# Kernel optimization log

Measured on AMD Instinct MI355X. Metric: run time of the kernel, lower is better.

Reference implementation:

```python
import jax, jax.numpy as jnp
import numpy as np

N_NODES = 50000


def gcn_conv(x, src, dst, W, b, n_nodes):
    """PyG-style GCNConv: x' = D^-1/2 (A + I) D^-1/2 (x W) + b.
    src/dst already include self-loops."""
    h = x @ W  # [N, C_out]
    # symmetric normalization from degree (with self-loops, unit edge weight)
    deg = jax.ops.segment_sum(jnp.ones_like(dst, dtype=h.dtype), dst,
                              num_segments=n_nodes)  # [N]
    dinv = jnp.where(deg > 0, jax.lax.rsqrt(deg), 0.0)
    norm = dinv[src] * dinv[dst]  # [E]
    msg = h[src] * norm[:, None]  # gather + scale, [E, C_out]
    out = jax.ops.segment_sum(msg, dst, num_segments=n_nodes)  # scatter-add
    return out + b


def setup_inputs() -> dict:
    key = jax.random.key(0)
    k1, k2, k3, k4, k5, k6 = jax.random.split(key, 6)
    in_c, hid_c, out_c = 128, 64, 64
    x = jax.random.normal(k1, (N_NODES, in_c), dtype=jnp.float32)
    edge_index = jax.random.randint(k2, (2, 800000), 0, N_NODES, dtype=jnp.int64)
    # Glorot-ish init for weights, zeros for bias (as PyG default)
    W1 = jax.random.normal(k3, (in_c, hid_c), dtype=jnp.float32) / np.sqrt(in_c)
    b1 = jnp.zeros((hid_c,), dtype=jnp.float32)
    W2 = jax.random.normal(k4, (hid_c, out_c), dtype=jnp.float32) / np.sqrt(hid_c)
    b2 = jnp.zeros((out_c,), dtype=jnp.float32)
    return {"x": x, "edge_index": edge_index, "W1": W1, "b1": b1,
            "W2": W2, "b2": b2}


def reference(x, edge_index, W1, b1, W2, b2):
    n = x.shape[0]
    loops = jnp.arange(n, dtype=edge_index.dtype)
    src = jnp.concatenate([edge_index[0], loops])  # add self-loops
    dst = jnp.concatenate([edge_index[1], loops])
    h = gcn_conv(x, src, dst, W1, b1, n)
    h = jax.nn.relu(h)
    return gcn_conv(h, src, dst, W2, b2, n)
```

## Files before the change

### kernel.cpp

```cpp
#include <hip/hip_runtime.h>
#include <hip/hip_fp16.h>


#define C_HID 64
#define NCHUNK 512
#define ES3 768
#define ES4 768

static inline size_t alignup(size_t x) { return (x + 255) & ~(size_t)255; }

typedef __attribute__((address_space(3))) unsigned int lds_uint;
typedef __attribute__((address_space(1))) const unsigned int glob_uint;

__device__ __forceinline__ int blockScanIncl256(int v, int* wsum) {
    const int lane = threadIdx.x & 63, wav = threadIdx.x >> 6;
    int s = v;
#pragma unroll
    for (int off = 1; off < 64; off <<= 1) {
        int t = __shfl_up(s, off);
        if (lane >= off) s += t;
    }
    if (lane == 63) wsum[wav] = s;
    __syncthreads();
    if (wav == 0 && lane < 4) {
        int ws = wsum[lane];
#pragma unroll
        for (int off = 1; off < 4; off <<= 1) {
            int t = __shfl_up(ws, off);
            if (lane >= off) ws += t;
        }
        wsum[lane] = ws;
    }
    __syncthreads();
    return (wav ? wsum[wav - 1] : 0) + s;
}

template <int K>
__global__ __launch_bounds__(256) void gemm1_hist_kernel(
    const float* __restrict__ X, const float* __restrict__ W,
    const int* __restrict__ dst, __half* __restrict__ outh,
    int* __restrict__ S, int n, int E, int ePer, int nb) {
    constexpr int KP = K + 4;
    __shared__ float Xs[64 * KP];
    __shared__ float Ws[K * 64];
    __shared__ int h[1024];
    const int t = threadIdx.x;
    const int lane = t & 63;
    const int wav = t >> 6;

    if ((int)blockIdx.x < NCHUNK) {
        for (int i = t; i < nb; i += 256) h[i] = 0;
        __syncthreads();
        int beg = blockIdx.x * ePer, end = min(E, beg + ePer);
        for (int e = beg + t; e < end; e += 256)
            atomicAdd(&h[dst[e] >> 6], 1);
        __syncthreads();
        for (int b = t; b < nb; b += 256)
            S[(size_t)b * NCHUNK + blockIdx.x] = h[b];
        return;
    }

    const int row0 = ((int)blockIdx.x - NCHUNK) * 64;
    {
        const char* gb = (const char*)W;
        char* lb = (char*)Ws;
        for (int off = wav * 1024; off < K * 64 * 4; off += 4096)
            __builtin_amdgcn_global_load_lds((glob_uint*)(gb + off + lane * 16),
                                             (lds_uint*)(lb + off), 16, 0, 0);
    }
    if (row0 + 64 <= n) {
        const float4* g4 = (const float4*)(X + (size_t)row0 * K);
        for (int i = t; i < 64 * (K / 4); i += 256) {
            float4 v = g4[i];
            int r = i / (K / 4), k0 = (i % (K / 4)) * 4;
            *(float4*)&Xs[r * KP + k0] = v;
        }
    } else {
        for (int i = t; i < 64 * K; i += 256) {
            int r = i / K, k = i % K;
            Xs[r * KP + k] = (row0 + r < n) ? X[(size_t)(row0 + r) * K + k] : 0.0f;
        }
    }
    __syncthreads();

    const int tx = t & 15;
    const int ty = t >> 4;
    float acc[4][4] = {{0.f}};
#pragma unroll 2
    for (int k0 = 0; k0 < K; k0 += 4) {
        float4 a0 = *(const float4*)&Xs[(4 * ty + 0) * KP + k0];
        float4 a1 = *(const float4*)&Xs[(4 * ty + 1) * KP + k0];
        float4 a2 = *(const float4*)&Xs[(4 * ty + 2) * KP + k0];
        float4 a3 = *(const float4*)&Xs[(4 * ty + 3) * KP + k0];
        float4 b0 = *(const float4*)&Ws[(k0 + 0) * 64 + 4 * tx];
        float4 b1 = *(const float4*)&Ws[(k0 + 1) * 64 + 4 * tx];
        float4 b2 = *(const float4*)&Ws[(k0 + 2) * 64 + 4 * tx];
        float4 b3 = *(const float4*)&Ws[(k0 + 3) * 64 + 4 * tx];
        const float* ap[4] = {(const float*)&a0, (const float*)&a1,
                              (const float*)&a2, (const float*)&a3};
        const float* bp[4] = {(const float*)&b0, (const float*)&b1,
                              (const float*)&b2, (const float*)&b3};
#pragma unroll
        for (int r = 0; r < 4; ++r)
#pragma unroll
            for (int kk = 0; kk < 4; ++kk) {
                float av = ap[r][kk];
#pragma unroll
                for (int c = 0; c < 4; ++c)
                    acc[r][c] = fmaf(av, bp[kk][c], acc[r][c]);
            }
    }
#pragma unroll
    for (int r = 0; r < 4; ++r) {
        int row = row0 + 4 * ty + r;
        if (row < n) {
            __half2 p01 = __floats2half2_rn(acc[r][0], acc[r][1]);
            __half2 p23 = __floats2half2_rn(acc[r][2], acc[r][3]);
            float2 st;
            ((__half2*)&st)[0] = p01;
            ((__half2*)&st)[1] = p23;
            *(float2*)&outh[(size_t)row * 64 + 4 * tx] = st;
        }
    }
}

__global__ __launch_bounds__(256) void scan_rows_kernel(
    int* __restrict__ S, int* __restrict__ T) {
    __shared__ int wsum[4];
    const int b = blockIdx.x, t = threadIdx.x;
    int4 v = make_int4(0, 0, 0, 0);
    if (t < NCHUNK / 4) v = ((const int4*)(S + (size_t)b * NCHUNK))[t];
    int p1 = v.x + v.y, p2 = p1 + v.z, p3 = p2 + v.w;
    int incl = blockScanIncl256(p3, wsum);
    int excl = incl - p3;
    if (t < NCHUNK / 4) {
        int4 o;
        o.x = excl; o.y = excl + v.x; o.z = excl + p1; o.w = excl + p2;
        ((int4*)(S + (size_t)b * NCHUNK))[t] = o;
    }
    if (t == 0) T[b] = wsum[3];
}

__global__ __launch_bounds__(256) void scatter_kernel(
    const int* __restrict__ src, const int* __restrict__ dst, int E, int ePer,
    const int* __restrict__ S, const int* __restrict__ T,
    unsigned* __restrict__ ebuf, int nb) {
    __shared__ int tmp[1024];
    __shared__ int arr[1024];
    __shared__ int wsum[4];
    const int b = blockIdx.x, t = threadIdx.x;
    {
        int a0 = (4 * t + 0 < nb) ? T[4 * t + 0] : 0;
        int a1 = (4 * t + 1 < nb) ? T[4 * t + 1] : 0;
        int a2 = (4 * t + 2 < nb) ? T[4 * t + 2] : 0;
        int a3 = (4 * t + 3 < nb) ? T[4 * t + 3] : 0;
        int p1 = a0 + a1, p2 = p1 + a2, p3 = p2 + a3;
        int incl = blockScanIncl256(p3, wsum);
        int excl = incl - p3;
        tmp[4 * t + 0] = excl;
        tmp[4 * t + 1] = excl + a0;
        tmp[4 * t + 2] = excl + p1;
        tmp[4 * t + 3] = excl + p2;
    }
    __syncthreads();
    for (int i = t; i < nb; i += 256)
        arr[i] = S[(size_t)i * NCHUNK + b] + tmp[i];
    __syncthreads();
    int beg = b * ePer, end = min(E, beg + ePer);
    for (int e = beg + t; e < end; e += 256) {
        int d = dst[e];
        int s = src[e];
        int pos = atomicAdd(&arr[d >> 6], 1);
        ebuf[pos] = ((unsigned)s << 6) | (unsigned)(d & 63);
    }
}

__global__ __launch_bounds__(256) void build_kernel(
    const unsigned* __restrict__ ebuf, const int* __restrict__ T,
    int* __restrict__ row_ptr, float* __restrict__ dinv,
    int* __restrict__ esrc, __half* __restrict__ g1, int n, int nb) {
    __shared__ int tmp[1024];
    __shared__ int cnt[64];
    __shared__ int cur[64];
    __shared__ float dvs[64];
    __shared__ int wsum[4];
    const int b = blockIdx.x, t = threadIdx.x;
    {
        int a0 = (4 * t + 0 < nb) ? T[4 * t + 0] : 0;
        int a1 = (4 * t + 1 < nb) ? T[4 * t + 1] : 0;
        int a2 = (4 * t + 2 < nb) ? T[4 * t + 2] : 0;
        int a3 = (4 * t + 3 < nb) ? T[4 * t + 3] : 0;
        int p1 = a0 + a1, p2 = p1 + a2, p3 = p2 + a3;
        int incl = blockScanIncl256(p3, wsum);
        int excl = incl - p3;
        tmp[4 * t + 0] = excl + a0;
        tmp[4 * t + 1] = excl + p1;
        tmp[4 * t + 2] = excl + p2;
        tmp[4 * t + 3] = excl + p3;
    }
    if (t < 64) cnt[t] = 0;
    __syncthreads();
    const int ebeg = b ? tmp[b - 1] : 0;
    const int eend = tmp[b];

    for (int e = ebeg + t; e < eend; e += 256)
        atomicAdd(&cnt[ebuf[e] & 63], 1);
    __syncthreads();
    if (t < 64) {
        int deg = cnt[t];
        int s = deg;
#pragma unroll
        for (int off = 1; off < 64; off <<= 1) {
            int x = __shfl_up(s, off);
            if (t >= off) s += x;
        }
        cur[t] = ebeg + s - deg;
        float dv = rsqrtf(1.0f + (float)deg);
        dvs[t] = dv;
        int v = (b << 6) + t;
        if (v < n) {
            row_ptr[v + 1] = ebeg + s;
            dinv[v] = dv;
            if (v == 0) row_ptr[0] = 0;
        }
    }
    __syncthreads();
    for (int e = ebeg + t; e < eend; e += 256) {
        unsigned p = ebuf[e];
        int pos = atomicAdd(&cur[p & 63], 1);
        esrc[pos] = (int)(p >> 6);
    }
    {
        const int row = t >> 2, q = t & 3;
        const int v = (b << 6) + row;
        if (v < n) {
            float dv = dvs[row];
            float4* gp = (float4*)(g1 + (size_t)v * 64 + q * 16);
            float4 r0 = gp[0], r1 = gp[1];
            __half2* h0 = (__half2*)&r0;
            __half2* h1 = (__half2*)&r1;
#pragma unroll
            for (int i2 = 0; i2 < 4; ++i2) {
                float2 f0 = __half22float2(h0[i2]);
                float2 f1 = __half22float2(h1[i2]);
                h0[i2] = __floats2half2_rn(f0.x * dv, f0.y * dv);
                h1[i2] = __floats2half2_rn(f1.x * dv, f1.y * dv);
            }
            gp[0] = r0;
            gp[1] = r1;
        }
    }
}

__device__ __forceinline__ void addf4(float acc[8], const float4& r) {
    const __half2* h = (const __half2*)&r;
#pragma unroll
    for (int q = 0; q < 4; ++q) {
        float2 f = __half22float2(h[q]);
        acc[2 * q] += f.x;
        acc[2 * q + 1] += f.y;
    }
}

template <bool LDSE>
__device__ __forceinline__ void agg8_body(
    const float4* __restrict__ hs4, const int* es, const int* __restrict__ esg,
    int beg0, int beg, int end, int c8, float acc[8]) {
    int j = beg;
    for (; j + 8 <= end; j += 8) {
        int s0, s1, s2, s3, s4, s5, s6, s7;
        if (LDSE) {
            s0 = es[j];     s1 = es[j + 1]; s2 = es[j + 2]; s3 = es[j + 3];
            s4 = es[j + 4]; s5 = es[j + 5]; s6 = es[j + 6]; s7 = es[j + 7];
        } else {
            const int* p = esg + beg0 + j;
            s0 = p[0]; s1 = p[1]; s2 = p[2]; s3 = p[3];
            s4 = p[4]; s5 = p[5]; s6 = p[6]; s7 = p[7];
        }
        float4 r0 = hs4[(size_t)s0 * 8 + c8];
        float4 r1 = hs4[(size_t)s1 * 8 + c8];
        float4 r2 = hs4[(size_t)s2 * 8 + c8];
        float4 r3 = hs4[(size_t)s3 * 8 + c8];
        float4 r4 = hs4[(size_t)s4 * 8 + c8];
        float4 r5 = hs4[(size_t)s5 * 8 + c8];
        float4 r6 = hs4[(size_t)s6 * 8 + c8];
        float4 r7 = hs4[(size_t)s7 * 8 + c8];
        addf4(acc, r0); addf4(acc, r1); addf4(acc, r2); addf4(acc, r3);
        addf4(acc, r4); addf4(acc, r5); addf4(acc, r6); addf4(acc, r7);
    }
    if (j + 4 <= end) {
        int s0, s1, s2, s3;
        if (LDSE) {
            s0 = es[j]; s1 = es[j + 1]; s2 = es[j + 2]; s3 = es[j + 3];
        } else {
            const int* p = esg + beg0 + j;
            s0 = p[0]; s1 = p[1]; s2 = p[2]; s3 = p[3];
        }
        float4 r0 = hs4[(size_t)s0 * 8 + c8];
        float4 r1 = hs4[(size_t)s1 * 8 + c8];
        float4 r2 = hs4[(size_t)s2 * 8 + c8];
        float4 r3 = hs4[(size_t)s3 * 8 + c8];
        addf4(acc, r0); addf4(acc, r1); addf4(acc, r2); addf4(acc, r3);
        j += 4;
    }
    for (; j < end; ++j) {
        int s0 = LDSE ? es[j] : esg[beg0 + j];
        float4 r0 = hs4[(size_t)s0 * 8 + c8];
        addf4(acc, r0);
    }
}

__global__ __launch_bounds__(256) void agg1_gemm2_kernel(
    const __half* __restrict__ g1, const int* __restrict__ row_ptr,
    const int* __restrict__ esrc, const float* __restrict__ dinv,
    const float* __restrict__ b1, const float* __restrict__ W2,
    __half* __restrict__ g2, int n) {
    __shared__ float Bt[32][68];
    __shared__ float Ws2[64 * 64];
    __shared__ int es[ES3];
    const int t = threadIdx.x, lane = t & 63, wav = t >> 6;
    const int row0 = blockIdx.x * 32;

    const int beg0 = row_ptr[row0];
    const int end0 = row_ptr[min(row0 + 32, n)];
    const int tot = end0 - beg0;
    const bool uselds = (tot <= ES3);
    if (uselds)
        for (int i = t; i < tot; i += 256) es[i] = esrc[beg0 + i];
    __syncthreads();

    {
        const char* gb = (const char*)W2;
        char* lb = (char*)Ws2;
        for (int off = wav * 1024; off < 64 * 64 * 4; off += 4096)
            __builtin_amdgcn_global_load_lds((glob_uint*)(gb + off + lane * 16),
                                             (lds_uint*)(lb + off), 16, 0, 0);
    }

    const int g = t >> 3;
    const int c8 = t & 7;
    const int v = row0 + g;
    const float4* __restrict__ hs4 = (const float4*)g1;

    if (v < n) {
        float acc[8];
        {
            float4 raw = hs4[(size_t)v * 8 + c8];
            const __half2* hp = (const __half2*)&raw;
#pragma unroll
            for (int q = 0; q < 4; ++q) {
                float2 f = __half22float2(hp[q]);
                acc[2 * q] = f.x; acc[2 * q + 1] = f.y;
            }
        }
        const int beg = row_ptr[v] - beg0;
        const int end = row_ptr[v + 1] - beg0;
        if (uselds) agg8_body<true>(hs4, es, esrc, beg0, beg, end, c8, acc);
        else        agg8_body<false>(hs4, es, esrc, beg0, beg, end, c8, acc);
        const float dv0 = dinv[v];
        const float* bb = b1 + c8 * 8;
        float4 w0, w1;
        w0.x = fmaxf(fmaf(acc[0], dv0, bb[0]), 0.f);
        w0.y = fmaxf(fmaf(acc[1], dv0, bb[1]), 0.f);
        w0.z = fmaxf(fmaf(acc[2], dv0, bb[2]), 0.f);
        w0.w = fmaxf(fmaf(acc[3], dv0, bb[3]), 0.f);
        w1.x = fmaxf(fmaf(acc[4], dv0, bb[4]), 0.f);
        w1.y = fmaxf(fmaf(acc[5], dv0, bb[5]), 0.f);
        w1.z = fmaxf(fmaf(acc[6], dv0, bb[6]), 0.f);
        w1.w = fmaxf(fmaf(acc[7], dv0, bb[7]), 0.f);
        *(float4*)&Bt[g][c8 * 8] = w0;
        *(float4*)&Bt[g][c8 * 8 + 4] = w1;
    } else {
        *(float4*)&Bt[g][c8 * 8] = make_float4(0.f, 0.f, 0.f, 0.f);
        *(float4*)&Bt[g][c8 * 8 + 4] = make_float4(0.f, 0.f, 0.f, 0.f);
    }
    __syncthreads();

    const int tx = t & 15;
    const int ty = t >> 4;
    float a2[2][4] = {{0.f}};
#pragma unroll 2
    for (int k0 = 0; k0 < 64; k0 += 4) {
        float4 x0 = *(const float4*)&Bt[2 * ty + 0][k0];
        float4 x1 = *(const float4*)&Bt[2 * ty + 1][k0];
        float4 w0 = *(const float4*)&Ws2[(k0 + 0) * 64 + 4 * tx];
        float4 w1 = *(const float4*)&Ws2[(k0 + 1) * 64 + 4 * tx];
        float4 w2 = *(const float4*)&Ws2[(k0 + 2) * 64 + 4 * tx];
        float4 w3 = *(const float4*)&Ws2[(k0 + 3) * 64 + 4 * tx];
        const float* xp[2] = {(const float*)&x0, (const float*)&x1};
        const float* wp[4] = {(const float*)&w0, (const float*)&w1,
                              (const float*)&w2, (const float*)&w3};
#pragma unroll
        for (int r = 0; r < 2; ++r)
#pragma unroll
            for (int kk = 0; kk < 4; ++kk) {
                float av = xp[r][kk];
#pragma unroll
                for (int cc = 0; cc < 4; ++cc)
                    a2[r][cc] = fmaf(av, wp[kk][cc], a2[r][cc]);
            }
    }
#pragma unroll
    for (int r = 0; r < 2; ++r) {
        int row = row0 + 2 * ty + r;
        if (row < n) {
            float dv = dinv[row];
            __half2 p01 = __floats2half2_rn(a2[r][0] * dv, a2[r][1] * dv);
            __half2 p23 = __floats2half2_rn(a2[r][2] * dv, a2[r][3] * dv);
            float2 st;
            ((__half2*)&st)[0] = p01;
            ((__half2*)&st)[1] = p23;
            *(float2*)&g2[(size_t)row * 64 + 4 * tx] = st;
        }
    }
}

__global__ __launch_bounds__(256) void aggregate2_kernel(
    const __half* __restrict__ hs,
    const int* __restrict__ row_ptr,
    const int* __restrict__ esrc,
    const float* __restrict__ dinv,
    const float* __restrict__ bias,
    float* __restrict__ out, int n) {
    __shared__ int es[ES4];
    const int t = threadIdx.x;
    const int row0 = blockIdx.x * 32;
    const int beg0 = row_ptr[row0];
    const int end0 = row_ptr[min(row0 + 32, n)];
    const int tot = end0 - beg0;
    const bool uselds = (tot <= ES4);
    if (uselds)
        for (int i = t; i < tot; i += 256) es[i] = esrc[beg0 + i];
    __syncthreads();

    const int v = row0 + (t >> 3);
    if (v >= n) return;
    const int c8 = t & 7;
    const float4* __restrict__ hs4 = (const float4*)hs;

    float acc[8];
    {
        float4 raw = hs4[(size_t)v * 8 + c8];
        const __half2* hp = (const __half2*)&raw;
#pragma unroll
        for (int q = 0; q < 4; ++q) {
            float2 f = __half22float2(hp[q]);
            acc[2 * q] = f.x; acc[2 * q + 1] = f.y;
        }
    }

    const int beg = row_ptr[v] - beg0;
    const int end = row_ptr[v + 1] - beg0;
    if (uselds) agg8_body<true>(hs4, es, esrc, beg0, beg, end, c8, acc);
    else        agg8_body<false>(hs4, es, esrc, beg0, beg, end, c8, acc);

    float dv = dinv[v];
    float4 b0 = *(const float4*)(bias + c8 * 8);
    float4 b1v = *(const float4*)(bias + c8 * 8 + 4);
    float4 o0, o1;
    o0.x = fmaf(acc[0], dv, b0.x); o0.y = fmaf(acc[1], dv, b0.y);
    o0.z = fmaf(acc[2], dv, b0.z); o0.w = fmaf(acc[3], dv, b0.w);
    o1.x = fmaf(acc[4], dv, b1v.x); o1.y = fmaf(acc[5], dv, b1v.y);
    o1.z = fmaf(acc[6], dv, b1v.z); o1.w = fmaf(acc[7], dv, b1v.w);
    float4* op = (float4*)(out + (size_t)v * 64 + c8 * 8);
    op[0] = o0;
    op[1] = o1;
}

extern "C" void kernel_launch(void* const* d_in, const int* in_sizes, int n_in,
                              void* d_out, int out_size, void* d_ws, size_t ws_size,
                              hipStream_t stream) {
    const float* x  = (const float*)d_in[0];
    const int*   ei = (const int*)d_in[1];
    const float* W1 = (const float*)d_in[2];
    const float* b1 = (const float*)d_in[3];
    const float* W2 = (const float*)d_in[4];
    const float* b2 = (const float*)d_in[5];
    float* out = (float*)d_out;

    const int C_IN = 128;
    const int n = in_sizes[0] / C_IN;
    const int E = in_sizes[1] / 2;
    const int* src = ei;
    const int* dst = ei + E;

    const int nb = (n + 63) >> 6;
    const int ngb = (n + 63) / 64;
    const int n32 = (n + 31) / 32;
    const int ePer = (E + NCHUNK - 1) / NCHUNK;

    char* w = (char*)d_ws;
    float*    dinv    = (float*)w;    w += alignup((size_t)n * sizeof(float));
    __half*   g1      = (__half*)w;   w += alignup((size_t)n * C_HID * sizeof(__half));
    __half*   g2      = (__half*)w;   w += alignup((size_t)n * C_HID * sizeof(__half));
    int*      row_ptr = (int*)w;      w += alignup((size_t)(n + 1) * sizeof(int));
    int*      S       = (int*)w;      w += alignup((size_t)nb * NCHUNK * sizeof(int));
    int*      T       = (int*)w;      w += alignup((size_t)(nb + 1) * sizeof(int));
    unsigned* ebuf    = (unsigned*)w; w += alignup((size_t)E * sizeof(unsigned));
    int*      esrc    = (int*)w;

    gemm1_hist_kernel<128><<<NCHUNK + ngb, 256, 0, stream>>>(
        x, W1, dst, g1, S, n, E, ePer, nb);

    scan_rows_kernel<<<nb, 256, 0, stream>>>(S, T);
    scatter_kernel<<<NCHUNK, 256, 0, stream>>>(src, dst, E, ePer, S, T, ebuf, nb);
    build_kernel<<<nb, 256, 0, stream>>>(ebuf, T, row_ptr, dinv, esrc, g1, n, nb);

    agg1_gemm2_kernel<<<n32, 256, 0, stream>>>(
        g1, row_ptr, esrc, dinv, b1, W2, g2, n);

    aggregate2_kernel<<<n32, 256, 0, stream>>>(
        g2, row_ptr, esrc, dinv, b2, out, n);
}
```

Before: 161.2 us.

## Build CSR with global per-node degree atomics and direct atomic scatter

Replaces the chunked two-level counting sort (per-chunk histograms, row scan, bucketed scatter into an intermediate buffer, then per-bucket local sort) with global per-node degree atomics in the histogram pass, a single build kernel that derives row_ptr and per-node cursors, and a direct scatter using global atomics on those cursors. It removes one kernel launch, the S matrix and the intermediate ebuf round trip. In exchange it adds a memset, many contended global atomics, and a nondeterministic edge order within each row, which can change floating-point summation order.

```diff
diff --git a/kernel.cpp b/kernel.cpp
--- a/kernel.cpp
+++ b/kernel.cpp
@@ -5,7 +5,6 @@
 #define C_HID 64
 #define NCHUNK 512
 #define ES3 768
-#define ES4 768
 
 static inline size_t alignup(size_t x) { return (x + 255) & ~(size_t)255; }
 
@@ -39,7 +38,8 @@
 __global__ __launch_bounds__(256) void gemm1_hist_kernel(
     const float* __restrict__ X, const float* __restrict__ W,
     const int* __restrict__ dst, __half* __restrict__ outh,
-    int* __restrict__ S, int n, int E, int ePer, int nb) {
+    int* __restrict__ deg, int* __restrict__ T,
+    int n, int E, int ePer, int nb) {
     constexpr int KP = K + 4;
     __shared__ float Xs[64 * KP];
     __shared__ float Ws[K * 64];
@@ -52,11 +52,16 @@
         for (int i = t; i < nb; i += 256) h[i] = 0;
         __syncthreads();
         int beg = blockIdx.x * ePer, end = min(E, beg + ePer);
-        for (int e = beg + t; e < end; e += 256)
-            atomicAdd(&h[dst[e] >> 6], 1);
+        for (int e = beg + t; e < end; e += 256) {
+            int d = dst[e];
+            atomicAdd(&deg[d], 1);
+            atomicAdd(&h[d >> 6], 1);
+        }
         __syncthreads();
-        for (int b = t; b < nb; b += 256)
-            S[(size_t)b * NCHUNK + blockIdx.x] = h[b];
+        for (int b = t; b < nb; b += 256) {
+            int c = h[b];
+            if (c) atomicAdd(&T[b], c);
+        }
         return;
     }
 
@@ -124,64 +129,11 @@
     }
 }
 
-__global__ __launch_bounds__(256) void scan_rows_kernel(
-    int* __restrict__ S, int* __restrict__ T) {
-    __shared__ int wsum[4];
-    const int b = blockIdx.x, t = threadIdx.x;
-    int4 v = make_int4(0, 0, 0, 0);
-    if (t < NCHUNK / 4) v = ((const int4*)(S + (size_t)b * NCHUNK))[t];
-    int p1 = v.x + v.y, p2 = p1 + v.z, p3 = p2 + v.w;
-    int incl = blockScanIncl256(p3, wsum);
-    int excl = incl - p3;
-    if (t < NCHUNK / 4) {
-        int4 o;
-        o.x = excl; o.y = excl + v.x; o.z = excl + p1; o.w = excl + p2;
-        ((int4*)(S + (size_t)b * NCHUNK))[t] = o;
-    }
-    if (t == 0) T[b] = wsum[3];
-}
-
-__global__ __launch_bounds__(256) void scatter_kernel(
-    const int* __restrict__ src, const int* __restrict__ dst, int E, int ePer,
-    const int* __restrict__ S, const int* __restrict__ T,
-    unsigned* __restrict__ ebuf, int nb) {
+__global__ __launch_bounds__(256) void build_kernel(
+    const int* __restrict__ deg, const int* __restrict__ T,
+    int* __restrict__ row_ptr, float* __restrict__ dinv, int* __restrict__ cur,
+    __half* __restrict__ g1, int n, int nb) {
     __shared__ int tmp[1024];
-    __shared__ int arr[1024];
-    __shared__ int wsum[4];
-    const int b = blockIdx.x, t = threadIdx.x;
-    {
-        int a0 = (4 * t + 0 < nb) ? T[4 * t + 0] : 0;
-        int a1 = (4 * t + 1 < nb) ? T[4 * t + 1] : 0;
-        int a2 = (4 * t + 2 < nb) ? T[4 * t + 2] : 0;
-        int a3 = (4 * t + 3 < nb) ? T[4 * t + 3] : 0;
-        int p1 = a0 + a1, p2 = p1 + a2, p3 = p2 + a3;
-        int incl = blockScanIncl256(p3, wsum);
-        int excl = incl - p3;
-        tmp[4 * t + 0] = excl;
-        tmp[4 * t + 1] = excl + a0;
-        tmp[4 * t + 2] = excl + p1;
-        tmp[4 * t + 3] = excl + p2;
-    }
-    __syncthreads();
-    for (int i = t; i < nb; i += 256)
-        arr[i] = S[(size_t)i * NCHUNK + b] + tmp[i];
-    __syncthreads();
-    int beg = b * ePer, end = min(E, beg + ePer);
-    for (int e = beg + t; e < end; e += 256) {
-        int d = dst[e];
-        int s = src[e];
-        int pos = atomicAdd(&arr[d >> 6], 1);
-        ebuf[pos] = ((unsigned)s << 6) | (unsigned)(d & 63);
-    }
-}
-
-__global__ __launch_bounds__(256) void build_kernel(
-    const unsigned* __restrict__ ebuf, const int* __restrict__ T,
-    int* __restrict__ row_ptr, float* __restrict__ dinv,
-    int* __restrict__ esrc, __half* __restrict__ g1, int n, int nb) {
-    __shared__ int tmp[1024];
-    __shared__ int cnt[64];
-    __shared__ int cur[64];
     __shared__ float dvs[64];
     __shared__ int wsum[4];
     const int b = blockIdx.x, t = threadIdx.x;
@@ -198,38 +150,28 @@
         tmp[4 * t + 2] = excl + p2;
         tmp[4 * t + 3] = excl + p3;
     }
-    if (t < 64) cnt[t] = 0;
     __syncthreads();
     const int ebeg = b ? tmp[b - 1] : 0;
-    const int eend = tmp[b];
-
-    for (int e = ebeg + t; e < eend; e += 256)
-        atomicAdd(&cnt[ebuf[e] & 63], 1);
-    __syncthreads();
+
     if (t < 64) {
-        int deg = cnt[t];
-        int s = deg;
+        const int v = (b << 6) + t;
+        int d = (v < n) ? deg[v] : 0;
+        int s = d;
 #pragma unroll
         for (int off = 1; off < 64; off <<= 1) {
             int x = __shfl_up(s, off);
             if (t >= off) s += x;
         }
-        cur[t] = ebeg + s - deg;
-        float dv = rsqrtf(1.0f + (float)deg);
+        float dv = rsqrtf(1.0f + (float)d);
         dvs[t] = dv;
-        int v = (b << 6) + t;
         if (v < n) {
             row_ptr[v + 1] = ebeg + s;
+            cur[v] = ebeg + s - d;
             dinv[v] = dv;
             if (v == 0) row_ptr[0] = 0;
         }
     }
     __syncthreads();
-    for (int e = ebeg + t; e < eend; e += 256) {
-        unsigned p = ebuf[e];
-        int pos = atomicAdd(&cur[p & 63], 1);
-        esrc[pos] = (int)(p >> 6);
-    }
     {
         const int row = t >> 2, q = t & 3;
         const int v = (b << 6) + row;
@@ -249,6 +191,18 @@
             gp[0] = r0;
             gp[1] = r1;
         }
+    }
+}
+
+__global__ __launch_bounds__(256) void scatter_kernel(
+    const int* __restrict__ src, const int* __restrict__ dst, int E,
+    int* __restrict__ cur, int* __restrict__ esrc) {
+    const int stride = gridDim.x * 256;
+    for (int e = blockIdx.x * 256 + threadIdx.x; e < E; e += stride) {
+        int d = dst[e];
+        int s = src[e];
+        int pos = atomicAdd(&cur[d], 1);
+        esrc[pos] = s;
     }
 }
 
@@ -422,13 +376,13 @@
     const float* __restrict__ dinv,
     const float* __restrict__ bias,
     float* __restrict__ out, int n) {
-    __shared__ int es[ES4];
+    __shared__ int es[ES3];
     const int t = threadIdx.x;
     const int row0 = blockIdx.x * 32;
     const int beg0 = row_ptr[row0];
     const int end0 = row_ptr[min(row0 + 32, n)];
     const int tot = end0 - beg0;
-    const bool uselds = (tot <= ES4);
+    const bool uselds = (tot <= ES3);
     if (uselds)
         for (int i = t; i < tot; i += 256) es[i] = esrc[beg0 + i];
     __syncthreads();
@@ -494,17 +448,20 @@
     __half*   g1      = (__half*)w;   w += alignup((size_t)n * C_HID * sizeof(__half));
     __half*   g2      = (__half*)w;   w += alignup((size_t)n * C_HID * sizeof(__half));
     int*      row_ptr = (int*)w;      w += alignup((size_t)(n + 1) * sizeof(int));
-    int*      S       = (int*)w;      w += alignup((size_t)nb * NCHUNK * sizeof(int));
-    int*      T       = (int*)w;      w += alignup((size_t)(nb + 1) * sizeof(int));
-    unsigned* ebuf    = (unsigned*)w; w += alignup((size_t)E * sizeof(unsigned));
+    int*      degT    = (int*)w;      w += alignup((size_t)(n + nb) * sizeof(int));
+    int*      cur     = (int*)w;      w += alignup((size_t)n * sizeof(int));
     int*      esrc    = (int*)w;
+    int* deg = degT;
+    int* T   = degT + n;
+
+    hipMemsetAsync(degT, 0, (size_t)(n + nb) * sizeof(int), stream);
 
     gemm1_hist_kernel<128><<<NCHUNK + ngb, 256, 0, stream>>>(
-        x, W1, dst, g1, S, n, E, ePer, nb);
-
-    scan_rows_kernel<<<nb, 256, 0, stream>>>(S, T);
-    scatter_kernel<<<NCHUNK, 256, 0, stream>>>(src, dst, E, ePer, S, T, ebuf, nb);
-    build_kernel<<<nb, 256, 0, stream>>>(ebuf, T, row_ptr, dinv, esrc, g1, n, nb);
+        x, W1, dst, g1, deg, T, n, E, ePer, nb);
+
+    build_kernel<<<nb, 256, 0, stream>>>(deg, T, row_ptr, dinv, cur, g1, n, nb);
+
+    scatter_kernel<<<1024, 256, 0, stream>>>(src, dst, E, cur, esrc);
 
     agg1_gemm2_kernel<<<n32, 256, 0, stream>>>(
         g1, row_ptr, esrc, dinv, b1, W2, g2, n);
```

After: 231.1 us. 43.3% more time.
